# Kernel optimization log

Hardware: AMD Instinct MI355X
Metric: run time of the kernel (lower is better)

## Reference

```python
import jax, jax.numpy as jnp
import numpy as np

N, D, E, R, G, M = 8192, 1024, 64, 64, 8, 8

def setup_inputs() -> dict:
    key = jax.random.key(0)
    k_h, k_wg, k_wl, k_w1, k_w2 = jax.random.split(key, 5)
    return {
        'h': jax.random.normal(k_h, (N, D), jnp.float32),
        'Wg': jax.random.normal(k_wg, (D, G), jnp.float32) * 0.02,  # nn.Linear weight (transposed)
        'bg': jnp.zeros((G,), jnp.float32),
        'Wloc': jax.random.normal(k_wl, (G, D, M), jnp.float32) * 0.02,
        'W1': jax.random.normal(k_w1, (E, D, R), jnp.float32) * 0.02,
        'W2': jax.random.normal(k_w2, (E, R, D), jnp.float32) * 0.02,
        'k': 2,
    }

def reference(h, Wg, bg, Wloc, W1, W2, k):
    n, d = h.shape
    g, _, m = Wloc.shape
    e = W1.shape[0]
    router_temp = 1.0
    # stage 1: group routing (top-1)
    g_scores = h @ Wg + bg                                   # (N, G)
    group_idx = jnp.argmax(g_scores, axis=-1)                # (N,)
    # stage 2: within-group scores; compute all groups (cheap: N*G*M) then select
    all_local = jnp.einsum('nd,gdm->ngm', h, Wloc)           # (N, G, M)
    local_scores = jnp.take_along_axis(all_local, group_idx[:, None, None], axis=1)[:, 0]  # (N, M)
    topv, topm = jax.lax.top_k(local_scores, k)              # (N, k)
    gate = jax.nn.softmax(topv / max(router_temp, 1e-6), axis=-1)
    expert_ids = group_idx[:, None] * m + topm               # (N, k) global expert ids
    # scatter gates into dense (N, E); topm entries are distinct per token
    gate_full = jnp.zeros((n, e), h.dtype).at[jnp.arange(n)[:, None], expert_ids].set(gate)
    # low-rank expert compute: relu(h @ W1) @ W2, weighted-combined
    tmp = jax.nn.relu(jnp.einsum('nd,edr->ner', h, W1))      # (N, E, R)
    out = jnp.einsum('ner,erd->nd', gate_full[:, :, None] * tmp, W2)  # (N, D)
    return out, expert_ids, gate, group_idx
```

## Files before the change

### kernel.cpp

```cpp
#include <hip/hip_runtime.h>
#include <hip/hip_bf16.h>
#include <cstdint>
#include <cstddef>

#define NTOK 8192
#define DIM  1024
#define NEXP 64
#define RANK 64
#define NGRP 8
#define NLOC 8

typedef __attribute__((ext_vector_type(8))) short bf16x8;
typedef __attribute__((ext_vector_type(4))) float f32x4;

static __device__ inline unsigned int pack_bf16x2(float a, float b) {
    __hip_bfloat16 ha = __float2bfloat16(a);
    __hip_bfloat16 hb = __float2bfloat16(b);
    return (unsigned int)(*(unsigned short*)&ha) |
           ((unsigned int)(*(unsigned short*)&hb) << 16);
}

__global__ __launch_bounds__(256, 4) void score_g_cast(
    const float* __restrict__ h, const float* __restrict__ Wg,
    const float* __restrict__ bg, unsigned short* __restrict__ hb,
    float* __restrict__ out_gidx, int* __restrict__ gidx_i,
    int* __restrict__ counts_g)
{
    __shared__ float Hs[16][66];
    __shared__ float Bs[64 * 8];
    __shared__ float Sp[16][16][8];
    __shared__ float Sg[16][9];
    __shared__ int   hist_g[NGRP];

    const int t0  = blockIdx.x * 16;
    const int tid = threadIdx.x;
    const int t   = tid & 15;
    const int kq  = tid >> 4;
    const int kbase = (kq >> 2) * 16 + (kq & 3);

    if (tid < NGRP) hist_g[tid] = 0;

    float acc[8] = {};
    for (int kc = 0; kc < DIM; kc += 64) {
        __syncthreads();
        {
            const int r = tid >> 4, c4 = tid & 15;
            const float4 v = *(const float4*)(h + (size_t)(t0 + r) * DIM + kc + c4 * 4);
            *(float2*)&Hs[r][c4 * 4]     = make_float2(v.x, v.y);
            *(float2*)&Hs[r][c4 * 4 + 2] = make_float2(v.z, v.w);
            uint2 pk;
            pk.x = pack_bf16x2(v.x, v.y);
            pk.y = pack_bf16x2(v.z, v.w);
            *(uint2*)(hb + (size_t)(t0 + r) * DIM + kc + c4 * 4) = pk;
        }
        {
            const float* src = Wg + (size_t)kc * NGRP;
            Bs[tid] = src[tid];
            Bs[tid + 256] = src[tid + 256];
        }
        __syncthreads();
#pragma unroll
        for (int kk = 0; kk < 4; ++kk) {
            const int k = kbase + kk * 4;
            const float a = Hs[t][k];
            const float4 b0 = *(const float4*)&Bs[k * 8];
            const float4 b1 = *(const float4*)&Bs[k * 8 + 4];
            acc[0] += a * b0.x; acc[1] += a * b0.y; acc[2] += a * b0.z; acc[3] += a * b0.w;
            acc[4] += a * b1.x; acc[5] += a * b1.y; acc[6] += a * b1.z; acc[7] += a * b1.w;
        }
    }
#pragma unroll
    for (int m = 0; m < 8; ++m) Sp[t][kq][m] = acc[m];
    __syncthreads();
    if (tid < 128) {
        const int tt = tid >> 3, m = tid & 7;
        float s = 0.f;
#pragma unroll
        for (int q = 0; q < 16; ++q) s += Sp[tt][q][m];
        Sg[tt][m] = s + bg[m];
    }
    __syncthreads();
    if (tid < 16) {
        int gi = 0; float best = Sg[tid][0];
#pragma unroll
        for (int g = 1; g < NGRP; ++g) {
            if (Sg[tid][g] > best) { best = Sg[tid][g]; gi = g; }
        }
        out_gidx[t0 + tid] = (float)gi;
        gidx_i[t0 + tid] = gi;
        atomicAdd(&hist_g[gi], 1);
    }
    __syncthreads();
    if (tid < NGRP) atomicAdd(&counts_g[tid], hist_g[tid]);
}

__global__ __launch_bounds__(256) void scatter_g(
    const int* __restrict__ gidx_i, const int* __restrict__ counts_g,
    int* __restrict__ cursor_g, int* __restrict__ glist)
{
    const int t = blockIdx.x * 256 + threadIdx.x;
    const int g = gidx_i[t];
    int base = 0;
    for (int gg = 0; gg < g; ++gg) base += counts_g[gg];
    const int pos = base + atomicAdd(&cursor_g[g], 1);
    glist[pos] = t;
}

__global__ __launch_bounds__(256, 4) void score_loc(
    const float* __restrict__ h, const float* __restrict__ Wloc,
    const int* __restrict__ counts_g, const int* __restrict__ glist,
    float* __restrict__ S_loc)
{
    __shared__ float Hs[16][66];
    __shared__ float Bs[64 * 8];
    __shared__ float Sp[16][16][8];
    __shared__ int   tokS[16];

    const int g = blockIdx.x;
    int base = 0;
    for (int gg = 0; gg < g; ++gg) base += counts_g[gg];
    const int ng = counts_g[g];
    const float* Wl = Wloc + (size_t)g * DIM * NLOC;
    const int tid = threadIdx.x;
    const int t   = tid & 15;
    const int kq  = tid >> 4;
    const int kbase = (kq >> 2) * 16 + (kq & 3);

    for (int tile = blockIdx.y; tile * 16 < ng; tile += gridDim.y) {
        __syncthreads();
        if (tid < 16) {
            const int gr = tile * 16 + tid;
            tokS[tid] = (gr < ng) ? glist[base + gr] : -1;
        }
        float acc[8] = {};
        for (int kc = 0; kc < DIM; kc += 64) {
            __syncthreads();
            {
                const int r = tid >> 4, c4 = tid & 15;
                const int tok = tokS[r];
                float4 v = make_float4(0.f, 0.f, 0.f, 0.f);
                if (tok >= 0)
                    v = *(const float4*)(h + (size_t)tok * DIM + kc + c4 * 4);
                *(float2*)&Hs[r][c4 * 4]     = make_float2(v.x, v.y);
                *(float2*)&Hs[r][c4 * 4 + 2] = make_float2(v.z, v.w);
            }
            {
                const float* src = Wl + (size_t)kc * NLOC;
                Bs[tid] = src[tid];
                Bs[tid + 256] = src[tid + 256];
            }
            __syncthreads();
#pragma unroll
            for (int kk = 0; kk < 4; ++kk) {
                const int k = kbase + kk * 4;
                const float a = Hs[t][k];
                const float4 b0 = *(const float4*)&Bs[k * 8];
                const float4 b1 = *(const float4*)&Bs[k * 8 + 4];
                acc[0] += a * b0.x; acc[1] += a * b0.y; acc[2] += a * b0.z; acc[3] += a * b0.w;
                acc[4] += a * b1.x; acc[5] += a * b1.y; acc[6] += a * b1.z; acc[7] += a * b1.w;
            }
        }
#pragma unroll
        for (int m = 0; m < 8; ++m) Sp[t][kq][m] = acc[m];
        __syncthreads();
        if (tid < 128) {
            const int tt = tid >> 3, m = tid & 7;
            const int tok = tokS[tt];
            if (tok >= 0) {
                float s = 0.f;
#pragma unroll
                for (int q = 0; q < 16; ++q) s += Sp[tt][q][m];
                S_loc[(size_t)tok * NLOC + m] = s;
            }
        }
    }
}

__global__ __launch_bounds__(256) void route2(
    const float* __restrict__ S_loc, const int* __restrict__ gidx_i,
    float* __restrict__ out_eid, float* __restrict__ out_gate,
    int* __restrict__ ws_eids, float* __restrict__ ws_gates,
    int* __restrict__ counts_e)
{
    __shared__ int hist[NEXP];
    if (threadIdx.x < NEXP) hist[threadIdx.x] = 0;
    __syncthreads();

    const int t = blockIdx.x * 256 + threadIdx.x;
    const int gi = gidx_i[t];
    float ls[NLOC];
    const float4 l0 = *(const float4*)(S_loc + (size_t)t * NLOC);
    const float4 l1 = *(const float4*)(S_loc + (size_t)t * NLOC + 4);
    ls[0] = l0.x; ls[1] = l0.y; ls[2] = l0.z; ls[3] = l0.w;
    ls[4] = l1.x; ls[5] = l1.y; ls[6] = l1.z; ls[7] = l1.w;

    int m1 = 0; float v1 = ls[0];
#pragma unroll
    for (int m = 1; m < NLOC; ++m) { if (ls[m] > v1) { v1 = ls[m]; m1 = m; } }
    int m2 = (m1 == 0) ? 1 : 0; float v2 = ls[m2];
#pragma unroll
    for (int m = 0; m < NLOC; ++m) {
        if (m != m1 && m != ((m1 == 0) ? 1 : 0) && ls[m] > v2) { v2 = ls[m]; m2 = m; }
    }
    const float e2v = expf(v2 - v1);
    const float inv = 1.f / (1.f + e2v);
    const float g0 = inv, g1 = e2v * inv;
    const int e0 = gi * NLOC + m1, e1 = gi * NLOC + m2;

    out_eid[t * 2 + 0] = (float)e0;
    out_eid[t * 2 + 1] = (float)e1;
    out_gate[t * 2 + 0] = g0;
    out_gate[t * 2 + 1] = g1;
    ws_eids[t * 2 + 0] = e0;
    ws_eids[t * 2 + 1] = e1;
    ws_gates[t * 2 + 0] = g0;
    ws_gates[t * 2 + 1] = g1;
    atomicAdd(&hist[e0], 1);
    atomicAdd(&hist[e1], 1);

    __syncthreads();
    if (threadIdx.x < NEXP) atomicAdd(&counts_e[threadIdx.x], hist[threadIdx.x]);
}

__global__ __launch_bounds__(64) void scan_kernel(
    const int* __restrict__ counts, int* __restrict__ offsets, int* __restrict__ cursor)
{
    const int e = threadIdx.x;
    const int c = counts[e];
    int s = c;
#pragma unroll
    for (int d = 1; d < 64; d <<= 1) {
        int v = __shfl_up(s, d, 64);
        if (e >= d) s += v;
    }
    offsets[e] = s - c;
    cursor[e] = s - c;
    if (e == 63) offsets[64] = s;
}

__global__ __launch_bounds__(256) void scatter_e(
    const int* __restrict__ ws_eids, const float* __restrict__ ws_gates,
    int* __restrict__ cursor, int* __restrict__ token_list, float* __restrict__ slot_gate)
{
    const int t = blockIdx.x * 256 + threadIdx.x;
    if (t >= NTOK) return;
#pragma unroll
    for (int j = 0; j < 2; ++j) {
        const int eid = ws_eids[t * 2 + j];
        const int pos = atomicAdd(&cursor[eid], 1);
        token_list[pos] = t * 2 + j;
        slot_gate[pos] = ws_gates[t * 2 + j];
    }
}

__global__ __launch_bounds__(256) void prep_w1(
    const float* __restrict__ W1, unsigned short* __restrict__ W1t)
{
    __shared__ float Ls[64][65];
    const int e = blockIdx.x, kb = blockIdx.y;
    const float* src = W1 + (size_t)e * DIM * RANK + (size_t)kb * 64 * RANK;
#pragma unroll
    for (int it = 0; it < 4; ++it) {
        const int kk = (threadIdx.x >> 4) + it * 16;
        const int rr = (threadIdx.x & 15) * 4;
        *(float4*)&Ls[kk][rr] = *(const float4*)(src + (size_t)kk * RANK + rr);
    }
    __syncthreads();
#pragma unroll
    for (int it = 0; it < 2; ++it) {
        const int idx = threadIdx.x + it * 256;
        const int r = idx >> 3, k8 = (idx & 7) * 8;
        uint4 v;
        v.x = pack_bf16x2(Ls[k8 + 0][r], Ls[k8 + 1][r]);
        v.y = pack_bf16x2(Ls[k8 + 2][r], Ls[k8 + 3][r]);
        v.z = pack_bf16x2(Ls[k8 + 4][r], Ls[k8 + 5][r]);
        v.w = pack_bf16x2(Ls[k8 + 6][r], Ls[k8 + 7][r]);
        *(uint4*)(W1t + (size_t)e * RANK * DIM + (size_t)r * DIM + kb * 64 + k8) = v;
    }
}

__global__ __launch_bounds__(256) void prep_w2(
    const float* __restrict__ W2, unsigned short* __restrict__ W2t)
{
    __shared__ float Ls[64][65];
    const int e = blockIdx.x, db = blockIdx.y;
    const float* src = W2 + (size_t)e * RANK * DIM + db * 64;
#pragma unroll
    for (int it = 0; it < 4; ++it) {
        const int rr = (threadIdx.x >> 4) + it * 16;
        const int dd = (threadIdx.x & 15) * 4;
        *(float4*)&Ls[rr][dd] = *(const float4*)(src + (size_t)rr * DIM + dd);
    }
    __syncthreads();
#pragma unroll
    for (int it = 0; it < 2; ++it) {
        const int idx = threadIdx.x + it * 256;
        const int d = idx >> 3, r8 = (idx & 7) * 8;
        uint4 v;
        v.x = pack_bf16x2(Ls[r8 + 0][d], Ls[r8 + 1][d]);
        v.y = pack_bf16x2(Ls[r8 + 2][d], Ls[r8 + 3][d]);
        v.z = pack_bf16x2(Ls[r8 + 4][d], Ls[r8 + 5][d]);
        v.w = pack_bf16x2(Ls[r8 + 6][d], Ls[r8 + 7][d]);
        *(uint4*)(W2t + (size_t)e * DIM * RANK + (size_t)(db * 64 + d) * RANK + r8) = v;
    }
}

__global__ __launch_bounds__(256, 2) void e1_mfma(
    const unsigned short* __restrict__ hb, const unsigned short* __restrict__ W1t,
    const int* __restrict__ offsets, const int* __restrict__ token_list,
    const float* __restrict__ slot_gate, unsigned short* __restrict__ P)
{
    __shared__ unsigned short Hs[64 * 72];
    __shared__ unsigned short Ws[64 * 72];
    __shared__ int   tokS[64];
    __shared__ float gateS[64];

    const int e  = blockIdx.x;
    const int n0 = offsets[e];
    const int ne = offsets[e + 1] - n0;
    const unsigned short* W1te = W1t + (size_t)e * RANK * DIM;
    const int tid  = threadIdx.x;
    const int wave = tid >> 6;
    const int lane = tid & 63;
    const int tx   = lane & 15;
    const int quad = lane >> 4;

    for (int tile = blockIdx.y; tile * 64 < ne; tile += 8) {
        const int row0 = tile * 64;
        __syncthreads();
        if (tid < 64) {
            const int gr = row0 + tid;
            tokS[tid]  = (gr < ne) ? token_list[n0 + gr] : -1;
            gateS[tid] = (gr < ne) ? slot_gate[n0 + gr] : 0.f;
        }
        f32x4 acc[4] = {};
        for (int kc = 0; kc < DIM; kc += 64) {
            __syncthreads();
#pragma unroll
            for (int it = 0; it < 2; ++it) {
                const int idx = tid + it * 256;
                const int s = idx >> 3, k8 = (idx & 7) * 8;
                const int ent = tokS[s];
                uint4 v = make_uint4(0, 0, 0, 0);
                if (ent >= 0)
                    v = *(const uint4*)(hb + (size_t)(ent >> 1) * DIM + kc + k8);
                *(uint4*)(Hs + s * 72 + k8) = v;
            }
#pragma unroll
            for (int it = 0; it < 2; ++it) {
                const int idx = tid + it * 256;
                const int r = idx >> 3, k8 = (idx & 7) * 8;
                *(uint4*)(Ws + r * 72 + k8) =
                    *(const uint4*)(W1te + (size_t)r * DIM + kc + k8);
            }
            __syncthreads();
#pragma unroll
            for (int ks = 0; ks < 2; ++ks) {
                const bf16x8 a = *(const bf16x8*)(Hs + (wave * 16 + tx) * 72 + ks * 32 + quad * 8);
#pragma unroll
                for (int j = 0; j < 4; ++j) {
                    const bf16x8 b = *(const bf16x8*)(Ws + (j * 16 + tx) * 72 + ks * 32 + quad * 8);
                    acc[j] = __builtin_amdgcn_mfma_f32_16x16x32_bf16(a, b, acc[j], 0, 0, 0);
                }
            }
        }
#pragma unroll
        for (int j = 0; j < 4; ++j) {
#pragma unroll
            for (int i = 0; i < 4; ++i) {
                const int sl = wave * 16 + quad * 4 + i;
                const int gr = row0 + sl;
                if (gr < ne) {
                    const float v = fmaxf(acc[j][i], 0.f) * gateS[sl];
                    __hip_bfloat16 hv = __float2bfloat16(v);
                    P[(size_t)(n0 + gr) * RANK + j * 16 + tx] = *(unsigned short*)&hv;
                }
            }
        }
    }
}

__global__ __launch_bounds__(256, 2) void e2_mfma(
    const unsigned short* __restrict__ P, const unsigned short* __restrict__ W2t,
    const int* __restrict__ offsets, const int* __restrict__ token_list,
    float* __restrict__ out, float* __restrict__ contrib)
{
    __shared__ unsigned short Ps[64 * 72];
    __shared__ unsigned short W2s[64 * 72];
    __shared__ int tokS[64];

    const int e = blockIdx.x;
    const int colbase = blockIdx.y * 64;
    const int n0 = offsets[e];
    const int ne = offsets[e + 1] - n0;
    const unsigned short* W2te = W2t + (size_t)e * DIM * RANK;
    const int tid  = threadIdx.x;
    const int wave = tid >> 6;
    const int lane = tid & 63;
    const int tx   = lane & 15;
    const int quad = lane >> 4;

#pragma unroll
    for (int it = 0; it < 2; ++it) {
        const int idx = tid + it * 256;
        const int d = idx >> 3, r8 = (idx & 7) * 8;
        *(uint4*)(W2s + d * 72 + r8) =
            *(const uint4*)(W2te + (size_t)(colbase + d) * RANK + r8);
    }

    for (int tile = blockIdx.z; tile * 64 < ne; tile += 4) {
        const int row0 = tile * 64;
        __syncthreads();
        if (tid < 64) {
            const int gr = row0 + tid;
            tokS[tid] = (gr < ne) ? token_list[n0 + gr] : -1;
        }
#pragma unroll
        for (int it = 0; it < 2; ++it) {
            const int idx = tid + it * 256;
            const int s = idx >> 3, r8 = (idx & 7) * 8;
            const int gr = row0 + s;
            uint4 v = make_uint4(0, 0, 0, 0);
            if (gr < ne) v = *(const uint4*)(P + (size_t)(n0 + gr) * RANK + r8);
            *(uint4*)(Ps + s * 72 + r8) = v;
        }
        __syncthreads();
        f32x4 acc[4] = {};
#pragma unroll
        for (int ks = 0; ks < 2; ++ks) {
            const bf16x8 a = *(const bf16x8*)(Ps + (wave * 16 + tx) * 72 + ks * 32 + quad * 8);
#pragma unroll
            for (int j = 0; j < 4; ++j) {
                const bf16x8 b = *(const bf16x8*)(W2s + (j * 16 + tx) * 72 + ks * 32 + quad * 8);
                acc[j] = __builtin_amdgcn_mfma_f32_16x16x32_bf16(a, b, acc[j], 0, 0, 0);
            }
        }
#pragma unroll
        for (int i = 0; i < 4; ++i) {
            const int sl = wave * 16 + quad * 4 + i;
            const int ent = tokS[sl];
            if (ent >= 0) {
                float* base = (ent & 1) ? contrib : out;
                float* op = base + (size_t)(ent >> 1) * DIM + colbase;
#pragma unroll
                for (int j = 0; j < 4; ++j)
                    op[j * 16 + tx] = acc[j][i];
            }
        }
    }
}

__global__ __launch_bounds__(256) void combine_kernel(
    const float* __restrict__ contrib, float* __restrict__ out)
{
    const size_t i = (size_t)blockIdx.x * 256 + threadIdx.x;
    float4 a = ((const float4*)out)[i];
    const float4 b = ((const float4*)contrib)[i];
    a.x += b.x; a.y += b.y; a.z += b.z; a.w += b.w;
    ((float4*)out)[i] = a;
}

extern "C" void kernel_launch(void* const* d_in, const int* in_sizes, int n_in,
                              void* d_out, int out_size, void* d_ws, size_t ws_size,
                              hipStream_t stream)
{
    const float* h    = (const float*)d_in[0];
    const float* Wg   = (const float*)d_in[1];
    const float* bg   = (const float*)d_in[2];
    const float* Wloc = (const float*)d_in[3];
    const float* W1   = (const float*)d_in[4];
    const float* W2   = (const float*)d_in[5];

    float* out_f    = (float*)d_out;
    float* out_main = out_f;
    float* out_eid  = out_f + (size_t)NTOK * DIM;
    float* out_gate = out_eid + (size_t)NTOK * 2;
    float* out_gidx = out_gate + (size_t)NTOK * 2;

    int* ws_i        = (int*)d_ws;
    int* counts_e    = ws_i;
    int* offsets_e   = ws_i + 64;
    int* cursor_e    = ws_i + 192;
    int* counts_g    = ws_i + 256;
    int* cursor_g    = ws_i + 264;
    int* gidx_i      = ws_i + 512;
    int* glist       = ws_i + 8704;
    int* ws_eids     = ws_i + 16896;
    int* token_list  = ws_i + 33280;
    float* ws_f      = (float*)(ws_i + 49664);
    float* ws_gates  = ws_f;
    float* slot_gate = ws_f + 16384;
    float* S_loc     = ws_f + 2 * 16384;
    unsigned short* P_h = (unsigned short*)(ws_f + 2 * 16384 + 65536);
    unsigned short* W1t = P_h + (size_t)16384 * RANK;
    unsigned short* W2t = W1t + (size_t)NEXP * RANK * DIM;
    float* contrib      = (float*)(W2t + (size_t)NEXP * DIM * RANK);
    unsigned short* hb = (unsigned short*)contrib;

    hipMemsetAsync(ws_i, 0, 272 * sizeof(int), stream);

    prep_w1<<<dim3(NEXP, 16), 256, 0, stream>>>(W1, W1t);
    prep_w2<<<dim3(NEXP, 16), 256, 0, stream>>>(W2, W2t);
    score_g_cast<<<NTOK / 16, 256, 0, stream>>>(h, Wg, bg, hb,
        out_gidx, gidx_i, counts_g);
    scatter_g<<<NTOK / 256, 256, 0, stream>>>(gidx_i, counts_g, cursor_g, glist);
    score_loc<<<dim3(NGRP, 64), 256, 0, stream>>>(h, Wloc, counts_g, glist, S_loc);
    route2<<<NTOK / 256, 256, 0, stream>>>(S_loc, gidx_i,
        out_eid, out_gate, ws_eids, ws_gates, counts_e);
    scan_kernel<<<1, 64, 0, stream>>>(counts_e, offsets_e, cursor_e);
    scatter_e<<<NTOK / 256, 256, 0, stream>>>(ws_eids, ws_gates, cursor_e,
        token_list, slot_gate);
    e1_mfma<<<dim3(NEXP, 8), 256, 0, stream>>>(hb, W1t, offsets_e, token_list,
        slot_gate, P_h);
    e2_mfma<<<dim3(NEXP, 16, 4), 256, 0, stream>>>(P_h, W2t, offsets_e, token_list,
        out_main, contrib);
    combine_kernel<<<(NTOK * DIM / 4) / 256, 256, 0, stream>>>(contrib, out_main);
}
```

Measured before the change: 269.5 us.

## Fuse group and local scoring with routing, merge weight prep, drop scan kernel

Folds the group-score, local-score and top-2 routing stages into one kernel per 16-token tile. Each token reads its chosen group's Wloc slice straight from global memory, so the group scatter list and the S_loc buffer are no longer needed. The two weight-transpose kernels become one launch, and the expert-offset scan is recomputed inside scatter_e, e1 and e2 instead of running as its own kernel. This removes several launches and intermediate passes over h. In exchange, h is read a second time per tile, Wloc access is gathered without shared-memory reuse, and counts_e takes global atomics per token.

```diff
diff --git a/kernel.cpp b/kernel.cpp
--- a/kernel.cpp
+++ b/kernel.cpp
@@ -20,25 +20,25 @@
            ((unsigned int)(*(unsigned short*)&hb) << 16);
 }
 
-__global__ __launch_bounds__(256, 4) void score_g_cast(
+__global__ __launch_bounds__(256, 4) void score_fused(
     const float* __restrict__ h, const float* __restrict__ Wg,
-    const float* __restrict__ bg, unsigned short* __restrict__ hb,
-    float* __restrict__ out_gidx, int* __restrict__ gidx_i,
-    int* __restrict__ counts_g)
+    const float* __restrict__ bg, const float* __restrict__ Wloc,
+    unsigned short* __restrict__ hb, float* __restrict__ out_gidx,
+    float* __restrict__ out_eid, float* __restrict__ out_gate,
+    int* __restrict__ ws_eids, float* __restrict__ ws_gates,
+    int* __restrict__ counts_e)
 {
     __shared__ float Hs[16][66];
     __shared__ float Bs[64 * 8];
     __shared__ float Sp[16][16][8];
     __shared__ float Sg[16][9];
-    __shared__ int   hist_g[NGRP];
+    __shared__ int   gsel[16];
 
     const int t0  = blockIdx.x * 16;
     const int tid = threadIdx.x;
     const int t   = tid & 15;
     const int kq  = tid >> 4;
     const int kbase = (kq >> 2) * 16 + (kq & 3);
-
-    if (tid < NGRP) hist_g[tid] = 0;
 
     float acc[8] = {};
     for (int kc = 0; kc < DIM; kc += 64) {
@@ -87,239 +87,183 @@
             if (Sg[tid][g] > best) { best = Sg[tid][g]; gi = g; }
         }
         out_gidx[t0 + tid] = (float)gi;
-        gidx_i[t0 + tid] = gi;
-        atomicAdd(&hist_g[gi], 1);
-    }
-    __syncthreads();
-    if (tid < NGRP) atomicAdd(&counts_g[tid], hist_g[tid]);
-}
-
-__global__ __launch_bounds__(256) void scatter_g(
-    const int* __restrict__ gidx_i, const int* __restrict__ counts_g,
-    int* __restrict__ cursor_g, int* __restrict__ glist)
-{
-    const int t = blockIdx.x * 256 + threadIdx.x;
-    const int g = gidx_i[t];
-    int base = 0;
-    for (int gg = 0; gg < g; ++gg) base += counts_g[gg];
-    const int pos = base + atomicAdd(&cursor_g[g], 1);
-    glist[pos] = t;
-}
-
-__global__ __launch_bounds__(256, 4) void score_loc(
-    const float* __restrict__ h, const float* __restrict__ Wloc,
-    const int* __restrict__ counts_g, const int* __restrict__ glist,
-    float* __restrict__ S_loc)
-{
-    __shared__ float Hs[16][66];
-    __shared__ float Bs[64 * 8];
-    __shared__ float Sp[16][16][8];
-    __shared__ int   tokS[16];
-
-    const int g = blockIdx.x;
-    int base = 0;
-    for (int gg = 0; gg < g; ++gg) base += counts_g[gg];
-    const int ng = counts_g[g];
-    const float* Wl = Wloc + (size_t)g * DIM * NLOC;
-    const int tid = threadIdx.x;
-    const int t   = tid & 15;
-    const int kq  = tid >> 4;
-    const int kbase = (kq >> 2) * 16 + (kq & 3);
-
-    for (int tile = blockIdx.y; tile * 16 < ng; tile += gridDim.y) {
-        __syncthreads();
-        if (tid < 16) {
-            const int gr = tile * 16 + tid;
-            tokS[tid] = (gr < ng) ? glist[base + gr] : -1;
-        }
-        float acc[8] = {};
-        for (int kc = 0; kc < DIM; kc += 64) {
-            __syncthreads();
-            {
-                const int r = tid >> 4, c4 = tid & 15;
-                const int tok = tokS[r];
-                float4 v = make_float4(0.f, 0.f, 0.f, 0.f);
-                if (tok >= 0)
-                    v = *(const float4*)(h + (size_t)tok * DIM + kc + c4 * 4);
-                *(float2*)&Hs[r][c4 * 4]     = make_float2(v.x, v.y);
-                *(float2*)&Hs[r][c4 * 4 + 2] = make_float2(v.z, v.w);
-            }
-            {
-                const float* src = Wl + (size_t)kc * NLOC;
-                Bs[tid] = src[tid];
-                Bs[tid + 256] = src[tid + 256];
-            }
-            __syncthreads();
+        gsel[tid] = gi;
+    }
+    __syncthreads();
+
+    {
+        const int gsel_t = gsel[t];
+        const float* wl = Wloc + (size_t)gsel_t * DIM * NLOC;
+        const float* hrow = h + (size_t)(t0 + t) * DIM;
+        float acc2[8] = {};
+        for (int kc = DIM - 64; kc >= 0; kc -= 64) {
+            const int k0 = kc + kq * 4;
+            const f32x4 hv = *(const f32x4*)(hrow + k0);
 #pragma unroll
             for (int kk = 0; kk < 4; ++kk) {
-                const int k = kbase + kk * 4;
-                const float a = Hs[t][k];
-                const float4 b0 = *(const float4*)&Bs[k * 8];
-                const float4 b1 = *(const float4*)&Bs[k * 8 + 4];
-                acc[0] += a * b0.x; acc[1] += a * b0.y; acc[2] += a * b0.z; acc[3] += a * b0.w;
-                acc[4] += a * b1.x; acc[5] += a * b1.y; acc[6] += a * b1.z; acc[7] += a * b1.w;
-            }
-        }
-#pragma unroll
-        for (int m = 0; m < 8; ++m) Sp[t][kq][m] = acc[m];
-        __syncthreads();
-        if (tid < 128) {
-            const int tt = tid >> 3, m = tid & 7;
-            const int tok = tokS[tt];
-            if (tok >= 0) {
-                float s = 0.f;
-#pragma unroll
-                for (int q = 0; q < 16; ++q) s += Sp[tt][q][m];
-                S_loc[(size_t)tok * NLOC + m] = s;
-            }
-        }
-    }
-}
-
-__global__ __launch_bounds__(256) void route2(
-    const float* __restrict__ S_loc, const int* __restrict__ gidx_i,
-    float* __restrict__ out_eid, float* __restrict__ out_gate,
-    int* __restrict__ ws_eids, float* __restrict__ ws_gates,
-    int* __restrict__ counts_e)
-{
-    __shared__ int hist[NEXP];
-    if (threadIdx.x < NEXP) hist[threadIdx.x] = 0;
-    __syncthreads();
-
-    const int t = blockIdx.x * 256 + threadIdx.x;
-    const int gi = gidx_i[t];
-    float ls[NLOC];
-    const float4 l0 = *(const float4*)(S_loc + (size_t)t * NLOC);
-    const float4 l1 = *(const float4*)(S_loc + (size_t)t * NLOC + 4);
-    ls[0] = l0.x; ls[1] = l0.y; ls[2] = l0.z; ls[3] = l0.w;
-    ls[4] = l1.x; ls[5] = l1.y; ls[6] = l1.z; ls[7] = l1.w;
-
-    int m1 = 0; float v1 = ls[0];
-#pragma unroll
-    for (int m = 1; m < NLOC; ++m) { if (ls[m] > v1) { v1 = ls[m]; m1 = m; } }
-    int m2 = (m1 == 0) ? 1 : 0; float v2 = ls[m2];
-#pragma unroll
-    for (int m = 0; m < NLOC; ++m) {
-        if (m != m1 && m != ((m1 == 0) ? 1 : 0) && ls[m] > v2) { v2 = ls[m]; m2 = m; }
-    }
-    const float e2v = expf(v2 - v1);
-    const float inv = 1.f / (1.f + e2v);
-    const float g0 = inv, g1 = e2v * inv;
-    const int e0 = gi * NLOC + m1, e1 = gi * NLOC + m2;
-
-    out_eid[t * 2 + 0] = (float)e0;
-    out_eid[t * 2 + 1] = (float)e1;
-    out_gate[t * 2 + 0] = g0;
-    out_gate[t * 2 + 1] = g1;
-    ws_eids[t * 2 + 0] = e0;
-    ws_eids[t * 2 + 1] = e1;
-    ws_gates[t * 2 + 0] = g0;
-    ws_gates[t * 2 + 1] = g1;
-    atomicAdd(&hist[e0], 1);
-    atomicAdd(&hist[e1], 1);
-
-    __syncthreads();
-    if (threadIdx.x < NEXP) atomicAdd(&counts_e[threadIdx.x], hist[threadIdx.x]);
-}
-
-__global__ __launch_bounds__(64) void scan_kernel(
-    const int* __restrict__ counts, int* __restrict__ offsets, int* __restrict__ cursor)
-{
-    const int e = threadIdx.x;
-    const int c = counts[e];
-    int s = c;
-#pragma unroll
-    for (int d = 1; d < 64; d <<= 1) {
-        int v = __shfl_up(s, d, 64);
-        if (e >= d) s += v;
-    }
-    offsets[e] = s - c;
-    cursor[e] = s - c;
-    if (e == 63) offsets[64] = s;
+                const float a = hv[kk];
+                const float4 b0 = *(const float4*)(wl + (size_t)(k0 + kk) * NLOC);
+                const float4 b1 = *(const float4*)(wl + (size_t)(k0 + kk) * NLOC + 4);
+                acc2[0] += a * b0.x; acc2[1] += a * b0.y; acc2[2] += a * b0.z; acc2[3] += a * b0.w;
+                acc2[4] += a * b1.x; acc2[5] += a * b1.y; acc2[6] += a * b1.z; acc2[7] += a * b1.w;
+            }
+        }
+#pragma unroll
+        for (int m = 0; m < 8; ++m) Sp[t][kq][m] = acc2[m];
+    }
+    __syncthreads();
+    if (tid < 128) {
+        const int tt = tid >> 3, m = tid & 7;
+        float s = 0.f;
+#pragma unroll
+        for (int q = 0; q < 16; ++q) s += Sp[tt][q][m];
+        Sg[tt][m] = s;
+    }
+    __syncthreads();
+
+    if (tid < 16) {
+        const int tok = t0 + tid;
+        float ls[NLOC];
+#pragma unroll
+        for (int m = 0; m < NLOC; ++m) ls[m] = Sg[tid][m];
+
+        int m1 = 0; float v1 = ls[0];
+#pragma unroll
+        for (int m = 1; m < NLOC; ++m) { if (ls[m] > v1) { v1 = ls[m]; m1 = m; } }
+        int m2 = (m1 == 0) ? 1 : 0; float v2 = ls[m2];
+#pragma unroll
+        for (int m = 0; m < NLOC; ++m) {
+            if (m != m1 && m != ((m1 == 0) ? 1 : 0) && ls[m] > v2) { v2 = ls[m]; m2 = m; }
+        }
+        const float e2v = expf(v2 - v1);
+        const float inv = 1.f / (1.f + e2v);
+        const float g0 = inv, g1 = e2v * inv;
+        const int gi = gsel[tid];
+        const int ea = gi * NLOC + m1, eb = gi * NLOC + m2;
+
+        out_eid[tok * 2 + 0] = (float)ea;
+        out_eid[tok * 2 + 1] = (float)eb;
+        out_gate[tok * 2 + 0] = g0;
+        out_gate[tok * 2 + 1] = g1;
+        ws_eids[tok * 2 + 0] = ea;
+        ws_eids[tok * 2 + 1] = eb;
+        ws_gates[tok * 2 + 0] = g0;
+        ws_gates[tok * 2 + 1] = g1;
+        atomicAdd(&counts_e[ea], 1);
+        atomicAdd(&counts_e[eb], 1);
+    }
 }
 
 __global__ __launch_bounds__(256) void scatter_e(
     const int* __restrict__ ws_eids, const float* __restrict__ ws_gates,
-    int* __restrict__ cursor, int* __restrict__ token_list, float* __restrict__ slot_gate)
-{
-    const int t = blockIdx.x * 256 + threadIdx.x;
+    const int* __restrict__ counts_e, int* __restrict__ cursor,
+    int* __restrict__ token_list, float* __restrict__ slot_gate)
+{
+    __shared__ int offS[64];
+    const int tid = threadIdx.x;
+    if (tid < 64) {
+        const int c = counts_e[tid];
+        int s = c;
+#pragma unroll
+        for (int d = 1; d < 64; d <<= 1) {
+            int v = __shfl_up(s, d, 64);
+            if (tid >= d) s += v;
+        }
+        offS[tid] = s - c;
+    }
+    __syncthreads();
+    const int t = blockIdx.x * 256 + tid;
     if (t >= NTOK) return;
 #pragma unroll
     for (int j = 0; j < 2; ++j) {
         const int eid = ws_eids[t * 2 + j];
-        const int pos = atomicAdd(&cursor[eid], 1);
+        const int pos = offS[eid] + atomicAdd(&cursor[eid], 1);
         token_list[pos] = t * 2 + j;
         slot_gate[pos] = ws_gates[t * 2 + j];
     }
 }
 
-__global__ __launch_bounds__(256) void prep_w1(
-    const float* __restrict__ W1, unsigned short* __restrict__ W1t)
+__global__ __launch_bounds__(256) void prep_w(
+    const float* __restrict__ W1, const float* __restrict__ W2,
+    unsigned short* __restrict__ W1t, unsigned short* __restrict__ W2t)
 {
     __shared__ float Ls[64][65];
-    const int e = blockIdx.x, kb = blockIdx.y;
-    const float* src = W1 + (size_t)e * DIM * RANK + (size_t)kb * 64 * RANK;
-#pragma unroll
-    for (int it = 0; it < 4; ++it) {
-        const int kk = (threadIdx.x >> 4) + it * 16;
-        const int rr = (threadIdx.x & 15) * 4;
-        *(float4*)&Ls[kk][rr] = *(const float4*)(src + (size_t)kk * RANK + rr);
-    }
-    __syncthreads();
-#pragma unroll
-    for (int it = 0; it < 2; ++it) {
-        const int idx = threadIdx.x + it * 256;
-        const int r = idx >> 3, k8 = (idx & 7) * 8;
-        uint4 v;
-        v.x = pack_bf16x2(Ls[k8 + 0][r], Ls[k8 + 1][r]);
-        v.y = pack_bf16x2(Ls[k8 + 2][r], Ls[k8 + 3][r]);
-        v.z = pack_bf16x2(Ls[k8 + 4][r], Ls[k8 + 5][r]);
-        v.w = pack_bf16x2(Ls[k8 + 6][r], Ls[k8 + 7][r]);
-        *(uint4*)(W1t + (size_t)e * RANK * DIM + (size_t)r * DIM + kb * 64 + k8) = v;
-    }
-}
-
-__global__ __launch_bounds__(256) void prep_w2(
-    const float* __restrict__ W2, unsigned short* __restrict__ W2t)
-{
-    __shared__ float Ls[64][65];
-    const int e = blockIdx.x, db = blockIdx.y;
-    const float* src = W2 + (size_t)e * RANK * DIM + db * 64;
-#pragma unroll
-    for (int it = 0; it < 4; ++it) {
-        const int rr = (threadIdx.x >> 4) + it * 16;
-        const int dd = (threadIdx.x & 15) * 4;
-        *(float4*)&Ls[rr][dd] = *(const float4*)(src + (size_t)rr * DIM + dd);
-    }
-    __syncthreads();
-#pragma unroll
-    for (int it = 0; it < 2; ++it) {
-        const int idx = threadIdx.x + it * 256;
-        const int d = idx >> 3, r8 = (idx & 7) * 8;
-        uint4 v;
-        v.x = pack_bf16x2(Ls[r8 + 0][d], Ls[r8 + 1][d]);
-        v.y = pack_bf16x2(Ls[r8 + 2][d], Ls[r8 + 3][d]);
-        v.z = pack_bf16x2(Ls[r8 + 4][d], Ls[r8 + 5][d]);
-        v.w = pack_bf16x2(Ls[r8 + 6][d], Ls[r8 + 7][d]);
-        *(uint4*)(W2t + (size_t)e * DIM * RANK + (size_t)(db * 64 + d) * RANK + r8) = v;
+    const int e = blockIdx.x;
+    const int y = blockIdx.y;
+    if (y < 16) {
+        const int kb = y;
+        const float* src = W1 + (size_t)e * DIM * RANK + (size_t)kb * 64 * RANK;
+#pragma unroll
+        for (int it = 0; it < 4; ++it) {
+            const int kk = (threadIdx.x >> 4) + it * 16;
+            const int rr = (threadIdx.x & 15) * 4;
+            *(float4*)&Ls[kk][rr] = *(const float4*)(src + (size_t)kk * RANK + rr);
+        }
+        __syncthreads();
+#pragma unroll
+        for (int it = 0; it < 2; ++it) {
+            const int idx = threadIdx.x + it * 256;
+            const int r = idx >> 3, k8 = (idx & 7) * 8;
+            uint4 v;
+            v.x = pack_bf16x2(Ls[k8 + 0][r], Ls[k8 + 1][r]);
+            v.y = pack_bf16x2(Ls[k8 + 2][r], Ls[k8 + 3][r]);
+            v.z = pack_bf16x2(Ls[k8 + 4][r], Ls[k8 + 5][r]);
+            v.w = pack_bf16x2(Ls[k8 + 6][r], Ls[k8 + 7][r]);
+            *(uint4*)(W1t + (size_t)e * RANK * DIM + (size_t)r * DIM + kb * 64 + k8) = v;
+        }
+    } else {
+        const int db = y - 16;
+        const float* src = W2 + (size_t)e * RANK * DIM + db * 64;
+#pragma unroll
+        for (int it = 0; it < 4; ++it) {
+            const int rr = (threadIdx.x >> 4) + it * 16;
+            const int dd = (threadIdx.x & 15) * 4;
+            *(float4*)&Ls[rr][dd] = *(const float4*)(src + (size_t)rr * DIM + dd);
+        }
+        __syncthreads();
+#pragma unroll
+        for (int it = 0; it < 2; ++it) {
+            const int idx = threadIdx.x + it * 256;
+            const int d = idx >> 3, r8 = (idx & 7) * 8;
+            uint4 v;
+            v.x = pack_bf16x2(Ls[r8 + 0][d], Ls[r8 + 1][d]);
+            v.y = pack_bf16x2(Ls[r8 + 2][d], Ls[r8 + 3][d]);
+            v.z = pack_bf16x2(Ls[r8 + 4][d], Ls[r8 + 5][d]);
+            v.w = pack_bf16x2(Ls[r8 + 6][d], Ls[r8 + 7][d]);
+            *(uint4*)(W2t + (size_t)e * DIM * RANK + (size_t)(db * 64 + d) * RANK + r8) = v;
+        }
     }
 }
 
 __global__ __launch_bounds__(256, 2) void e1_mfma(
     const unsigned short* __restrict__ hb, const unsigned short* __restrict__ W1t,
-    const int* __restrict__ offsets, const int* __restrict__ token_list,
+    const int* __restrict__ counts_e, const int* __restrict__ token_list,
     const float* __restrict__ slot_gate, unsigned short* __restrict__ P)
 {
     __shared__ unsigned short Hs[64 * 72];
     __shared__ unsigned short Ws[64 * 72];
     __shared__ int   tokS[64];
     __shared__ float gateS[64];
-
-    const int e  = blockIdx.x;
-    const int n0 = offsets[e];
-    const int ne = offsets[e + 1] - n0;
+    __shared__ int   offS[65];
+
+    const int e   = blockIdx.x;
+    const int tid = threadIdx.x;
+    if (tid < 64) {
+        const int c = counts_e[tid];
+        int s = c;
+#pragma unroll
+        for (int d = 1; d < 64; d <<= 1) {
+            int v = __shfl_up(s, d, 64);
+            if (tid >= d) s += v;
+        }
+        offS[tid] = s - c;
+        if (tid == 63) offS[64] = s;
+    }
+    __syncthreads();
+    const int n0 = offS[e];
+    const int ne = offS[e + 1] - n0;
+
     const unsigned short* W1te = W1t + (size_t)e * RANK * DIM;
-    const int tid  = threadIdx.x;
     const int wave = tid >> 6;
     const int lane = tid & 63;
     const int tx   = lane & 15;
@@ -382,19 +326,33 @@
 
 __global__ __launch_bounds__(256, 2) void e2_mfma(
     const unsigned short* __restrict__ P, const unsigned short* __restrict__ W2t,
-    const int* __restrict__ offsets, const int* __restrict__ token_list,
+    const int* __restrict__ counts_e, const int* __restrict__ token_list,
     float* __restrict__ out, float* __restrict__ contrib)
 {
     __shared__ unsigned short Ps[64 * 72];
     __shared__ unsigned short W2s[64 * 72];
     __shared__ int tokS[64];
+    __shared__ int offS[65];
 
     const int e = blockIdx.x;
     const int colbase = blockIdx.y * 64;
-    const int n0 = offsets[e];
-    const int ne = offsets[e + 1] - n0;
+    const int tid = threadIdx.x;
+    if (tid < 64) {
+        const int c = counts_e[tid];
+        int s = c;
+#pragma unroll
+        for (int d = 1; d < 64; d <<= 1) {
+            int v = __shfl_up(s, d, 64);
+            if (tid >= d) s += v;
+        }
+        offS[tid] = s - c;
+        if (tid == 63) offS[64] = s;
+    }
+    __syncthreads();
+    const int n0 = offS[e];
+    const int ne = offS[e + 1] - n0;
+
     const unsigned short* W2te = W2t + (size_t)e * DIM * RANK;
-    const int tid  = threadIdx.x;
     const int wave = tid >> 6;
     const int lane = tid & 63;
     const int tx   = lane & 15;
@@ -479,40 +437,28 @@
 
     int* ws_i        = (int*)d_ws;
     int* counts_e    = ws_i;
-    int* offsets_e   = ws_i + 64;
     int* cursor_e    = ws_i + 192;
-    int* counts_g    = ws_i + 256;
-    int* cursor_g    = ws_i + 264;
-    int* gidx_i      = ws_i + 512;
-    int* glist       = ws_i + 8704;
     int* ws_eids     = ws_i + 16896;
     int* token_list  = ws_i + 33280;
     float* ws_f      = (float*)(ws_i + 49664);
     float* ws_gates  = ws_f;
     float* slot_gate = ws_f + 16384;
-    float* S_loc     = ws_f + 2 * 16384;
     unsigned short* P_h = (unsigned short*)(ws_f + 2 * 16384 + 65536);
     unsigned short* W1t = P_h + (size_t)16384 * RANK;
     unsigned short* W2t = W1t + (size_t)NEXP * RANK * DIM;
     float* contrib      = (float*)(W2t + (size_t)NEXP * DIM * RANK);
     unsigned short* hb = (unsigned short*)contrib;
 
-    hipMemsetAsync(ws_i, 0, 272 * sizeof(int), stream);
-
-    prep_w1<<<dim3(NEXP, 16), 256, 0, stream>>>(W1, W1t);
-    prep_w2<<<dim3(NEXP, 16), 256, 0, stream>>>(W2, W2t);
-    score_g_cast<<<NTOK / 16, 256, 0, stream>>>(h, Wg, bg, hb,
-        out_gidx, gidx_i, counts_g);
-    scatter_g<<<NTOK / 256, 256, 0, stream>>>(gidx_i, counts_g, cursor_g, glist);
-    score_loc<<<dim3(NGRP, 64), 256, 0, stream>>>(h, Wloc, counts_g, glist, S_loc);
-    route2<<<NTOK / 256, 256, 0, stream>>>(S_loc, gidx_i,
-        out_eid, out_gate, ws_eids, ws_gates, counts_e);
-    scan_kernel<<<1, 64, 0, stream>>>(counts_e, offsets_e, cursor_e);
-    scatter_e<<<NTOK / 256, 256, 0, stream>>>(ws_eids, ws_gates, cursor_e,
-        token_list, slot_gate);
-    e1_mfma<<<dim3(NEXP, 8), 256, 0, stream>>>(hb, W1t, offsets_e, token_list,
+    hipMemsetAsync(ws_i, 0, 256 * sizeof(int), stream);
+
+    prep_w<<<dim3(NEXP, 32), 256, 0, stream>>>(W1, W2, W1t, W2t);
+    score_fused<<<NTOK / 16, 256, 0, stream>>>(h, Wg, bg, Wloc, hb,
+        out_gidx, out_eid, out_gate, ws_eids, ws_gates, counts_e);
+    scatter_e<<<NTOK / 256, 256, 0, stream>>>(ws_eids, ws_gates, counts_e,
+        cursor_e, token_list, slot_gate);
+    e1_mfma<<<dim3(NEXP, 8), 256, 0, stream>>>(hb, W1t, counts_e, token_list,
         slot_gate, P_h);
-    e2_mfma<<<dim3(NEXP, 16, 4), 256, 0, stream>>>(P_h, W2t, offsets_e, token_list,
+    e2_mfma<<<dim3(NEXP, 16, 4), 256, 0, stream>>>(P_h, W2t, counts_e, token_list,
         out_main, contrib);
     combine_kernel<<<(NTOK * DIM / 4) / 256, 256, 0, stream>>>(contrib, out_main);
 }
```

Result: faster. 263.7 us (-2.2%).
